# Kernel optimization log

Measured on AMD Instinct MI355X. Metric: run time of the kernel, lower is better.

## Reference

```python
import jax, jax.numpy as jnp
import numpy as np
from jax import lax

D_MODEL = 1024
EXPAND = 2
D_INNER = EXPAND * D_MODEL          # 2048
HEADDIM = 64
NHEADS = D_INNER // HEADDIM         # 32
D_STATE = 128
D_CONV = 4
NGROUPS = 1
CONV_DIM = D_INNER + 2 * NGROUPS * D_STATE   # 2304
D_IN_PROJ = 2 * D_INNER + 2 * NGROUPS * D_STATE + NHEADS  # 4384
EPS = 1e-5
BSZ, SEQ = 4, 1024


def _layer_norm(x):
    mu = jnp.mean(x, -1, keepdims=True)
    v = jnp.var(x, -1, keepdims=True)
    return (x - mu) * lax.rsqrt(v + EPS)


def _smart_flip(X, mask):
    # reverse only the non-padded prefix of each sequence
    B, L, _ = X.shape
    lengths = jnp.sum(~mask, axis=1)                     # (B,)
    r = jnp.arange(L)[None, :]                           # (1,L)
    pos = jnp.where(r < lengths[:, None], lengths[:, None] - 1 - r, r)
    return jnp.take_along_axis(X, pos[:, :, None], axis=1)


def _mamba2(u, in_proj_w, conv_w, conv_b, dt_bias, A_log, D, norm_w, out_proj_w):
    B, L, _ = u.shape
    zxbcdt = jnp.einsum('bld,ed->ble', u, in_proj_w)     # (B,L,D_IN_PROJ)
    z = zxbcdt[..., :D_INNER]
    xBC = zxbcdt[..., D_INNER:D_INNER + CONV_DIM]
    dt = zxbcdt[..., D_INNER + CONV_DIM:]                # (B,L,H)
    dt = jax.nn.softplus(dt + dt_bias)
    # causal depthwise conv1d over time, then SiLU
    xc = jnp.transpose(xBC, (0, 2, 1))                   # (B,C,L)
    xc = jnp.pad(xc, ((0, 0), (0, 0), (D_CONV - 1, 0)))
    xc = lax.conv_general_dilated(xc, conv_w.reshape(CONV_DIM, 1, D_CONV), (1,), 'VALID',
                                  feature_group_count=CONV_DIM)
    xBC = jax.nn.silu(jnp.transpose(xc + conv_b[None, :, None], (0, 2, 1)))
    x = xBC[..., :D_INNER].reshape(B, L, NHEADS, HEADDIM)
    Bmat = xBC[..., D_INNER:D_INNER + D_STATE]           # (B,L,N)  (ngroups=1)
    Cmat = xBC[..., D_INNER + D_STATE:]                  # (B,L,N)
    A = -jnp.exp(A_log)                                  # (H,)
    dA = jnp.exp(dt * A)                                 # (B,L,H)

    def step(h, inp):
        dA_t, dt_t, x_t, B_t, C_t = inp
        # h: (B,H,P,N)
        h = h * dA_t[:, :, None, None] + (dt_t[:, :, None] * x_t)[..., None] * B_t[:, None, None, :]
        y = jnp.einsum('bhpn,bn->bhp', h, C_t)
        return h, y

    h0 = jnp.zeros((B, NHEADS, HEADDIM, D_STATE), u.dtype)
    xs = (jnp.moveaxis(dA, 1, 0), jnp.moveaxis(dt, 1, 0), jnp.moveaxis(x, 1, 0),
          jnp.moveaxis(Bmat, 1, 0), jnp.moveaxis(Cmat, 1, 0))
    _, ys = lax.scan(step, h0, xs)                       # (L,B,H,P)
    y = jnp.moveaxis(ys, 0, 1) + D[None, None, :, None] * x
    y = y.reshape(B, L, D_INNER)
    g = y * jax.nn.silu(z)                               # gated RMSNorm (norm_before_gate=False)
    y = g * lax.rsqrt(jnp.mean(g * g, -1, keepdims=True) + EPS) * norm_w
    return jnp.einsum('ble,de->bld', y, out_proj_w)


def setup_inputs() -> dict:
    key = jax.random.key(0)
    ks = jax.random.split(key, 16)
    dt_f = jax.random.uniform(ks[4], (NHEADS,), minval=0.001, maxval=0.1)
    dt_r = jax.random.uniform(ks[10], (NHEADS,), minval=0.001, maxval=0.1)
    inv_softplus = lambda d: d + jnp.log(-jnp.expm1(-d))
    return {
        'hidden_states': jax.random.normal(ks[0], (BSZ, SEQ, D_MODEL), jnp.float32),
        'src_key_padding_mask': jnp.zeros((BSZ, SEQ), jnp.bool_),
        'in_proj_w': jax.random.normal(ks[1], (D_IN_PROJ, D_MODEL), jnp.float32) / np.sqrt(D_MODEL),
        'out_proj_w': jax.random.normal(ks[2], (D_MODEL, D_INNER), jnp.float32) / np.sqrt(D_INNER),
        'conv_w_f': jax.random.normal(ks[3], (CONV_DIM, D_CONV), jnp.float32) / np.sqrt(D_CONV),
        'conv_b_f': jnp.zeros((CONV_DIM,), jnp.float32),
        'dt_bias_f': inv_softplus(dt_f),
        'A_log_f': jnp.log(jax.random.uniform(ks[5], (NHEADS,), minval=1.0, maxval=16.0)),
        'D_f': jnp.ones((NHEADS,), jnp.float32),
        'norm_w_f': jnp.ones((D_INNER,), jnp.float32),
        'conv_w_r': jax.random.normal(ks[9], (CONV_DIM, D_CONV), jnp.float32) / np.sqrt(D_CONV),
        'conv_b_r': jnp.zeros((CONV_DIM,), jnp.float32),
        'dt_bias_r': inv_softplus(dt_r),
        'A_log_r': jnp.log(jax.random.uniform(ks[11], (NHEADS,), minval=1.0, maxval=16.0)),
        'D_r': jnp.ones((NHEADS,), jnp.float32),
        'norm_w_r': jnp.ones((D_INNER,), jnp.float32),
    }


def reference(hidden_states, src_key_padding_mask, in_proj_w, out_proj_w,
              conv_w_f, conv_b_f, dt_bias_f, A_log_f, D_f, norm_w_f,
              conv_w_r, conv_b_r, dt_bias_r, A_log_r, D_r, norm_w_r):
    h = _layer_norm(hidden_states)
    out = _mamba2(h, in_proj_w, conv_w_f, conv_b_f, dt_bias_f, A_log_f, D_f, norm_w_f, out_proj_w)
    rev = _smart_flip(h, src_key_padding_mask)
    out_rev = _mamba2(rev, in_proj_w, conv_w_r, conv_b_r, dt_bias_r, A_log_r, D_r, norm_w_r, out_proj_w)
    out_rev = _smart_flip(out_rev, src_key_padding_mask)
    out = (out + out_rev) / 2
    return _layer_norm(out)
```

## Files before the change

kernel.cpp:

```cpp
#include <hip/hip_runtime.h>


#define BSZ 4
#define SEQ 1024
#define DMODEL 1024
#define DINNER 2048
#define NHEADS 32
#define HEADDIM 64
#define DSTATE 128
#define CONVDIM 2304
#define DPROJ 4384
#define DPROJ_PAD 4480
#define NTOK (BSZ*SEQ)
#define EPSF 1e-5f
#define CH 32
#define NCHK (SEQ/CH)

typedef float f32x4 __attribute__((ext_vector_type(4)));
typedef __bf16 bf16x8 __attribute__((ext_vector_type(8)));
typedef __bf16 bf16x4 __attribute__((ext_vector_type(4)));

__device__ __forceinline__ unsigned short f2bf(float f) {
  unsigned int x = __float_as_uint(f);
  unsigned int r = (x + 0x7fffu + ((x >> 16) & 1u)) >> 16;
  return (unsigned short)r;
}
__device__ __forceinline__ float bf2f(unsigned short u) {
  return __uint_as_float(((unsigned int)u) << 16);
}

__device__ __forceinline__ void async_load16(const void* g, void* l) {
  __builtin_amdgcn_global_load_lds(
      (const __attribute__((address_space(1))) void*)g,
      (__attribute__((address_space(3))) void*)l, 16, 0, 0);
}

#define W1N (DPROJ_PAD * DMODEL)
#define W2N (DMODEL * DINNER)
__global__ void k_convert(const float* __restrict__ w1, const float* __restrict__ w2,
                          unsigned short* __restrict__ o1, unsigned short* __restrict__ o2) {
  int idx = blockIdx.x * 256 + threadIdx.x;
  if (idx < W1N) {
    int row = idx >> 10, col = idx & 1023;
    float v = (row < DPROJ) ? w1[(size_t)row * DMODEL + col] : 0.f;
    o1[idx] = f2bf(v);
  } else {
    int k = idx - W1N;
    o2[k] = f2bf(w2[k]);
  }
}
__global__ void k_lengths(const unsigned char* __restrict__ mask, int* __restrict__ lengths) {
  int b = blockIdx.x, tid = threadIdx.x;
  int cnt = 0;
  for (int k = 0; k < 4; ++k)
    cnt += (mask[(size_t)b * SEQ + tid + k * 256] == 0) ? 1 : 0;
  for (int o = 32; o > 0; o >>= 1) cnt += __shfl_down(cnt, o);
  __shared__ int red[4];
  if ((tid & 63) == 0) red[tid >> 6] = cnt;
  __syncthreads();
  if (tid == 0) lengths[b] = red[0] + red[1] + red[2] + red[3];
}

__global__ __launch_bounds__(256) void k_ln_bf16(const float* __restrict__ in,
                                                 unsigned short* __restrict__ out) {
  int row = blockIdx.x, tid = threadIdx.x;
  float4 v = ((const float4*)(in + (size_t)row * DMODEL))[tid];
  float s = v.x + v.y + v.z + v.w;
  float ss = v.x * v.x + v.y * v.y + v.z * v.z + v.w * v.w;
  for (int o = 32; o > 0; o >>= 1) { s += __shfl_down(s, o); ss += __shfl_down(ss, o); }
  __shared__ float red[8];
  if ((tid & 63) == 0) { red[tid >> 6] = s; red[4 + (tid >> 6)] = ss; }
  __syncthreads();
  s = red[0] + red[1] + red[2] + red[3];
  ss = red[4] + red[5] + red[6] + red[7];
  float mu = s * (1.f / DMODEL);
  float var = ss * (1.f / DMODEL) - mu * mu;
  float rs = rsqrtf(var + EPSF);
  ushort4 o;
  o.x = f2bf((v.x - mu) * rs); o.y = f2bf((v.y - mu) * rs);
  o.z = f2bf((v.z - mu) * rs); o.w = f2bf((v.w - mu) * rs);
  ((ushort4*)(out + (size_t)row * DMODEL))[tid] = o;
}

__global__ __launch_bounds__(256) void k_ln_out(const unsigned short* __restrict__ in,
                                                float* __restrict__ out) {
  int row = blockIdx.x, tid = threadIdx.x;
  ushort4 u = ((const ushort4*)(in + (size_t)row * DMODEL))[tid];
  float4 v;
  v.x = bf2f(u.x); v.y = bf2f(u.y); v.z = bf2f(u.z); v.w = bf2f(u.w);
  float s = v.x + v.y + v.z + v.w;
  float ss = v.x * v.x + v.y * v.y + v.z * v.z + v.w * v.w;
  for (int o = 32; o > 0; o >>= 1) { s += __shfl_down(s, o); ss += __shfl_down(ss, o); }
  __shared__ float red[8];
  if ((tid & 63) == 0) { red[tid >> 6] = s; red[4 + (tid >> 6)] = ss; }
  __syncthreads();
  s = red[0] + red[1] + red[2] + red[3];
  ss = red[4] + red[5] + red[6] + red[7];
  float mu = s * (1.f / DMODEL);
  float var = ss * (1.f / DMODEL) - mu * mu;
  float rs = rsqrtf(var + EPSF);
  float4 o;
  o.x = (v.x - mu) * rs; o.y = (v.y - mu) * rs;
  o.z = (v.z - mu) * rs; o.w = (v.w - mu) * rs;
  ((float4*)(out + (size_t)row * DMODEL))[tid] = o;
}

__global__ __launch_bounds__(256) void k_gemm_bt_h(const unsigned short* __restrict__ A,
                                                   const unsigned short* __restrict__ B,
                                                   unsigned short* __restrict__ C,
                                                   int K, int lda, int ldb, int ldc) {
  __shared__ unsigned short Asm[2][128 * 32];
  __shared__ unsigned short Bsm[2][128 * 32];
  const int tid = threadIdx.x;
  const int lane = tid & 63;
  const int w = tid >> 6;
  const int wm = w >> 1, wn = w & 1;
  const long m0 = (long)blockIdx.x * 128;
  const long n0 = (long)blockIdx.y * 128;

  const int sr = lane >> 2;
  const int sc = (lane & 3) * 8;
  const unsigned short* gA0 = A + (m0 + (w * 2 + 0) * 16 + sr) * (long)lda + sc;
  const unsigned short* gA1 = A + (m0 + (w * 2 + 1) * 16 + sr) * (long)lda + sc;
  const unsigned short* gB0 = B + (n0 + (w * 2 + 0) * 16 + sr) * (long)ldb + sc;
  const unsigned short* gB1 = B + (n0 + (w * 2 + 1) * 16 + sr) * (long)ldb + sc;

  f32x4 acc[4][4] = {};
  const int q8 = (lane >> 4) * 8;
  const int r16 = lane & 15;

  for (int k0 = 0; k0 < K; k0 += 64) {
#pragma unroll
    for (int h = 0; h < 2; ++h) {
      const int ko = k0 + h * 32;
      async_load16(gA0 + ko, Asm[h] + (w * 2 + 0) * 512);
      async_load16(gA1 + ko, Asm[h] + (w * 2 + 1) * 512);
      async_load16(gB0 + ko, Bsm[h] + (w * 2 + 0) * 512);
      async_load16(gB1 + ko, Bsm[h] + (w * 2 + 1) * 512);
    }
    __syncthreads();
#pragma unroll
    for (int h = 0; h < 2; ++h) {
      bf16x8 af[4], bfr[4];
#pragma unroll
      for (int i = 0; i < 4; ++i)
        af[i] = *reinterpret_cast<const bf16x8*>(Asm[h] + (wm * 64 + i * 16 + r16) * 32 + q8);
#pragma unroll
      for (int j = 0; j < 4; ++j)
        bfr[j] = *reinterpret_cast<const bf16x8*>(Bsm[h] + (wn * 64 + j * 16 + r16) * 32 + q8);
#pragma unroll
      for (int i = 0; i < 4; ++i)
#pragma unroll
        for (int j = 0; j < 4; ++j)
          acc[i][j] = __builtin_amdgcn_mfma_f32_16x16x32_bf16(af[i], bfr[j], acc[i][j], 0, 0, 0);
    }
    __syncthreads();
  }
  const int q = lane >> 4, cn = lane & 15;
#pragma unroll
  for (int i = 0; i < 4; ++i)
#pragma unroll
    for (int j = 0; j < 4; ++j) {
      long crow = m0 + wm * 64 + i * 16 + q * 4;
      long ccol = n0 + wn * 64 + j * 16 + cn;
#pragma unroll
      for (int r = 0; r < 4; ++r)
        C[(crow + r) * (long)ldc + ccol] = f2bf(acc[i][j][r]);
    }
}

__global__ __launch_bounds__(256) void k_conv(
    const __bf16* __restrict__ zxb,
    const float* __restrict__ cw_f, const float* __restrict__ cb_f,
    const float* __restrict__ cw_r, const float* __restrict__ cb_r,
    const int* __restrict__ lengths,
    __bf16* __restrict__ xb) {
  const int bx = blockIdx.x;
  const int tg = bx & 63;
  const int db = bx >> 6;
  const int b = db & 3;
  const int dir = db >> 2;
  const int tid = threadIdx.x;
  const int len = lengths[b];
  const int t0 = tg * 16;

  const float* cw = dir ? cw_r : cw_f;
  const float* cb = dir ? cb_r : cb_f;

  float w0[9], w1[9], w2[9], w3[9], bias[9];
  float r0[9], r1[9], r2[9], r3[9];
#pragma unroll
  for (int k = 0; k < 9; ++k) {
    int c = tid + k * 256;
    float4 w4 = *(const float4*)(cw + (size_t)c * 4);
    w0[k] = w4.x; w1[k] = w4.y; w2[k] = w4.z; w3[k] = w4.w;
    bias[k] = cb[c];
    r0[k] = 0.f; r1[k] = 0.f; r2[k] = 0.f;
  }
  auto rowptr = [&](int tt) -> const __bf16* {
    int s = dir ? ((tt < len) ? (len - 1 - tt) : tt) : tt;
    return zxb + ((size_t)b * SEQ + s) * DPROJ_PAD + DINNER;
  };
  if (t0 >= 3) {
    const __bf16* ra = rowptr(t0 - 3);
    const __bf16* rb = rowptr(t0 - 2);
    const __bf16* rc = rowptr(t0 - 1);
#pragma unroll
    for (int k = 0; k < 9; ++k) {
      int c = tid + k * 256;
      r0[k] = (float)ra[c]; r1[k] = (float)rb[c]; r2[k] = (float)rc[c];
    }
  }
  {
    const __bf16* rp = rowptr(t0);
#pragma unroll
    for (int k = 0; k < 9; ++k) r3[k] = (float)rp[tid + k * 256];
  }
  for (int j = 0; j < 16; ++j) {
    float r4[9];
    if (j < 15) {
      const __bf16* rp = rowptr(t0 + j + 1);
#pragma unroll
      for (int k = 0; k < 9; ++k) r4[k] = (float)rp[tid + k * 256];
    }
    __bf16* orow = xb + ((size_t)db * SEQ + t0 + j) * CONVDIM;
#pragma unroll
    for (int k = 0; k < 9; ++k) {
      float acc = bias[k];
      acc = fmaf(w0[k], r0[k], acc);
      acc = fmaf(w1[k], r1[k], acc);
      acc = fmaf(w2[k], r2[k], acc);
      acc = fmaf(w3[k], r3[k], acc);
      float sig = 1.f / (1.f + __expf(-acc));
      orow[tid + k * 256] = (__bf16)(acc * sig);
      r0[k] = r1[k]; r1[k] = r2[k]; r2[k] = r3[k]; r3[k] = r4[k];
    }
  }
}

__global__ __launch_bounds__(256) void k_dtprep(
    const __bf16* __restrict__ zxb,
    const float* __restrict__ dtb_f, const float* __restrict__ dtb_r,
    const float* __restrict__ al_f, const float* __restrict__ al_r,
    const int* __restrict__ lengths, float* __restrict__ ddg) {
  const int task = (blockIdx.x * 256 + threadIdx.x) >> 5;
  const int l32 = threadIdx.x & 31;
  const int chunk = task & 31, hh = (task >> 5) & 31, db = task >> 10;
  const int b = db & 3, dir = db >> 2;
  const int len = lengths[b];
  const float dtbv = (dir ? dtb_r : dtb_f)[hh];
  const float Ah = -__expf((dir ? al_r : al_f)[hh]);
  const int s = chunk * 32 + l32;
  const int sf = dir ? ((s < len) ? (len - 1 - s) : s) : s;
  float raw = (float)zxb[(size_t)(b * SEQ + sf) * DPROJ_PAD + DINNER + CONVDIM + hh] + dtbv;
  float d = (raw > 20.f) ? raw : log1pf(__expf(raw));
  float cum = d;
#pragma unroll
  for (int o = 1; o < 32; o <<= 1) {
    float v = __shfl_up(cum, o, 32);
    if (l32 >= o) cum += v;
  }
  float cum31 = __shfl(cum, 31, 32);
  float* o = ddg + (size_t)task * 128;
  o[l32]      = d;
  o[32 + l32] = Ah * cum;
  o[64 + l32] = d * __expf(Ah * (cum31 - cum));
  o[96 + l32] = __expf(Ah * cum);
}

__global__ __launch_bounds__(256, 2) void k_scan(
    const __bf16* __restrict__ xb, const float* __restrict__ ddg,
    const float* __restrict__ D_f, const float* __restrict__ D_r,
    unsigned short* __restrict__ y) {
  __shared__ __bf16 Crawf[4096];
  __shared__ __bf16 Brawf[4096];
  __shared__ __bf16 Braw2[4096];
  __shared__ __bf16 BTf[4096];
  __shared__ float  ddL[2][128];
  __shared__ __bf16 SL[1024];
  __shared__ __bf16 HL[4][2048];

  const int bx = blockIdx.x;
  const int h = bx & 31;
  const int db = bx >> 5;
  const int dir = db >> 2;
  const int tid = threadIdx.x;
  const int lane = tid & 63;
  const int w = tid >> 6;
  const int l15 = lane & 15;
  const int q = lane >> 4;

  const float Dh = (dir ? D_r : D_f)[h];
  const __bf16* xbase = xb + (size_t)db * SEQ * CONVDIM;
  const float* ddbase = ddg + (size_t)bx * NCHK * 128;
  unsigned short* ybase = y + (size_t)db * SEQ * DINNER + h * HEADDIM;

  for (int i = lane; i < 2048; i += 64) HL[w][i] = (__bf16)0.f;
  for (int i = tid; i < 1024; i += 256) SL[i] = (__bf16)0.f;

  f32x4 accH[8] = {};

  auto issue = [&](int c, int nb) {
    const __bf16* xr = xbase + (size_t)c * CH * CONVDIM;
#pragma unroll
    for (int k = 0; k < 2; ++k) {
      const int idx = w * 2 + k;
      const int P = idx * 64 + lane;
      const int tt = P >> 8, kk = (P >> 6) & 3, qq = (P >> 4) & 3, ll = P & 15;
      const __bf16* gB = xr + (size_t)(tt * 16 + ll) * CONVDIM + DINNER + kk * 32 + qq * 8;
      async_load16(gB, &Brawf[idx * 512]);
      async_load16(gB + 128, &Crawf[idx * 512]);
      const int s = P >> 4, n8 = P & 15;
      const __bf16* g2 = xr + (size_t)s * CONVDIM + DINNER + n8 * 8;
      async_load16(g2, &Braw2[idx * 512]);
    }
    if (w == 3 && lane < 32)
      async_load16(ddbase + (size_t)c * 128 + lane * 4, &ddL[nb][0]);
  };

  auto load_xt = [&](int c) {
    bf16x8 v;
    const __bf16* gx = xbase + (size_t)(c * CH + q * 8) * CONVDIM + h * HEADDIM + w * 16 + l15;
#pragma unroll
    for (int j = 0; j < 8; ++j) v[j] = gx[(size_t)j * CONVDIM];
    return v;
  };

  issue(0, 0);
  bf16x8 xt = load_xt(0);
  __syncthreads();

  for (int c = 0; c < NCHK; ++c) {
    const int cb = c & 1, nb = cb ^ 1;

    {
      const int n = tid & 127, sg = tid >> 7;
#pragma unroll
      for (int e = 0; e < 2; ++e) {
        const int qp = sg * 2 + e;
        bf16x8 v;
#pragma unroll
        for (int j = 0; j < 8; ++j) v[j] = Braw2[(qp * 8 + j) * 128 + n];
        *(bf16x8*)&BTf[((n >> 4) * 64 + qp * 16 + (n & 15)) * 8] = v;
      }
    }

    bf16x8 Cf0[4], Cf1[4];
#pragma unroll
    for (int kk = 0; kk < 4; ++kk) {
      Cf0[kk] = *(const bf16x8*)&Crawf[(kk * 64 + lane) * 8];
      Cf1[kk] = *(const bf16x8*)&Crawf[((4 + kk) * 64 + lane) * 8];
    }
    if (w < 3) {
      const int tt = (w == 0) ? 0 : 1;
      const int ss = (w == 2) ? 1 : 0;
      f32x4 G = {};
#pragma unroll
      for (int kk = 0; kk < 4; ++kk) {
        bf16x8 Bq = *(const bf16x8*)&Brawf[((ss * 4 + kk) * 64 + lane) * 8];
        G = __builtin_amdgcn_mfma_f32_16x16x32_bf16(Bq, tt ? Cf1[kk] : Cf0[kk], G, 0, 0, 0);
      }
      const float cdt = ddL[cb][32 + tt * 16 + l15];
      f32x4 sdt4 = *(const f32x4*)&ddL[cb][ss * 16 + q * 4];
      f32x4 cds4 = *(const f32x4*)&ddL[cb][32 + ss * 16 + q * 4];
      bf16x4 sv;
#pragma unroll
      for (int r = 0; r < 4; ++r) {
        const int s0 = q * 4 + r;
        float v = G[r] * sdt4[r] * __expf(cdt - cds4[r]);
        if (tt == ss) {
          if (l15 < s0) v = 0.f;
          else if (l15 == s0) v += Dh;
        }
        sv[r] = (__bf16)v;
      }
      *(bf16x4*)&SL[tt * 512 + (ss * 2 + (q >> 1)) * 128 + l15 * 8 + (q & 1) * 4] = sv;
    }
    __syncthreads();

    if (c + 1 < NCHK) issue(c + 1, nb);
    bf16x8 xt_n;
    if (c + 1 < NCHK) xt_n = load_xt(c + 1);

    f32x4 accy0 = {}, accy1 = {};
    {
      bf16x8 S0 = *(const bf16x8*)&SL[lane * 8];
      bf16x8 S1 = *(const bf16x8*)&SL[(64 + lane) * 8];
      accy0 = __builtin_amdgcn_mfma_f32_16x16x32_bf16(S0, xt, accy0, 0, 0, 0);
      accy1 = __builtin_amdgcn_mfma_f32_16x16x32_bf16(S1, xt, accy1, 0, 0, 0);
    }
    {
      f32x4 ai0 = {}, ai1 = {};
#pragma unroll
      for (int kk = 0; kk < 4; ++kk) {
        bf16x8 Hf = *(const bf16x8*)&HL[w][(kk * 64 + lane) * 8];
        ai0 = __builtin_amdgcn_mfma_f32_16x16x32_bf16(Cf0[kk], Hf, ai0, 0, 0, 0);
        ai1 = __builtin_amdgcn_mfma_f32_16x16x32_bf16(Cf1[kk], Hf, ai1, 0, 0, 0);
      }
      f32x4 P0 = *(const f32x4*)&ddL[cb][96 + q * 4];
      f32x4 P1 = *(const f32x4*)&ddL[cb][96 + 16 + q * 4];
      accy0 = accy0 + ai0 * P0;
      accy1 = accy1 + ai1 * P1;
    }
    {
      const float atot = ddL[cb][96 + 31];
      bf16x8 xw;
#pragma unroll
      for (int j = 0; j < 8; ++j)
        xw[j] = (__bf16)((float)xt[j] * ddL[cb][64 + q * 8 + j]);
#pragma unroll
      for (int nt = 0; nt < 8; ++nt) {
        bf16x8 Bt = *(const bf16x8*)&BTf[(nt * 64 + lane) * 8];
        accH[nt] = accH[nt] * atot;
        accH[nt] = __builtin_amdgcn_mfma_f32_16x16x32_bf16(Bt, xw, accH[nt], 0, 0, 0);
      }
#pragma unroll
      for (int nt = 0; nt < 8; ++nt) {
        const int n0 = nt * 16 + q * 4;
        bf16x4 hv;
#pragma unroll
        for (int r = 0; r < 4; ++r) hv[r] = (__bf16)accH[nt][r];
        *(bf16x4*)&HL[w][(n0 >> 5) * 512 + ((n0 >> 3) & 3) * 128 + l15 * 8 + (n0 & 7)] = hv;
      }
    }
#pragma unroll
    for (int r = 0; r < 4; ++r) {
      ybase[(size_t)(c * CH + q * 4 + r) * DINNER + w * 16 + l15] = f2bf(accy0[r]);
      ybase[(size_t)(c * CH + 16 + q * 4 + r) * DINNER + w * 16 + l15] = f2bf(accy1[r]);
    }
    xt = xt_n;
    __syncthreads();
  }
}

__global__ __launch_bounds__(256) void k_gate_combine(
    const __bf16* __restrict__ zxb, const unsigned short* __restrict__ y,
    const float* __restrict__ nw_f, const float* __restrict__ nw_r,
    const int* __restrict__ lengths, unsigned short* __restrict__ comb) {
  const int bx = blockIdx.x;
  const int b = bx >> 10, l = bx & 1023;
  const int tid = threadIdx.x;
  const int len = lengths[b];
  const int pos = (l < len) ? (len - 1 - l) : l;
  const __bf16* z = zxb + (size_t)bx * DPROJ_PAD;
  const unsigned short* yf = y + ((size_t)b * SEQ + l) * DINNER;
  const unsigned short* yr = y + ((size_t)(BSZ + b) * SEQ + pos) * DINNER;

  float gf[8], gr[8];
  float sf = 0.f, sr = 0.f;
#pragma unroll
  for (int k = 0; k < 8; ++k) {
    int c = tid + k * 256;
    float zz = (float)z[c];
    float sz = zz / (1.f + __expf(-zz));
    float vf = bf2f(yf[c]) * sz;
    float vr = bf2f(yr[c]) * sz;
    gf[k] = vf; gr[k] = vr;
    sf += vf * vf; sr += vr * vr;
  }
  for (int o = 32; o > 0; o >>= 1) { sf += __shfl_down(sf, o); sr += __shfl_down(sr, o); }
  __shared__ float red[8];
  if ((tid & 63) == 0) { red[tid >> 6] = sf; red[4 + (tid >> 6)] = sr; }
  __syncthreads();
  sf = red[0] + red[1] + red[2] + red[3];
  sr = red[4] + red[5] + red[6] + red[7];
  float rf = rsqrtf(sf * (1.f / DINNER) + EPSF);
  float rr = rsqrtf(sr * (1.f / DINNER) + EPSF);
#pragma unroll
  for (int k = 0; k < 8; ++k) {
    int c = tid + k * 256;
    float o = 0.5f * (gf[k] * rf * nw_f[c] + gr[k] * rr * nw_r[c]);
    comb[(size_t)bx * DINNER + c] = f2bf(o);
  }
}

extern "C" void kernel_launch(void* const* d_in, const int* in_sizes, int n_in,
                              void* d_out, int out_size, void* d_ws, size_t ws_size,
                              hipStream_t stream) {
  const float* hidden      = (const float*)d_in[0];
  const unsigned char* msk = (const unsigned char*)d_in[1];
  const float* in_proj_w   = (const float*)d_in[2];
  const float* out_proj_w  = (const float*)d_in[3];
  const float* conv_w_f    = (const float*)d_in[4];
  const float* conv_b_f    = (const float*)d_in[5];
  const float* dt_bias_f   = (const float*)d_in[6];
  const float* A_log_f     = (const float*)d_in[7];
  const float* D_f         = (const float*)d_in[8];
  const float* norm_w_f    = (const float*)d_in[9];
  const float* conv_w_r    = (const float*)d_in[10];
  const float* conv_b_r    = (const float*)d_in[11];
  const float* dt_bias_r   = (const float*)d_in[12];
  const float* A_log_r     = (const float*)d_in[13];
  const float* D_r         = (const float*)d_in[14];
  const float* norm_w_r    = (const float*)d_in[15];
  float* outF = (float*)d_out;

  char* ws = (char*)d_ws;
  size_t o_w1b  = 0;
  size_t o_w2b  = o_w1b  + 9175040;
  size_t o_hb   = o_w2b  + 4194304;
  size_t o_zx   = o_hb   + 8388608;
  size_t o_xb   = o_zx   + 36700160;
  size_t o_dd   = o_xb   + 37748736;
  size_t o_y    = o_dd   + 4194304;
  size_t o_comb = o_y    + 33554432;
  size_t o_outp = o_comb + 16777216;
  size_t o_len  = o_outp + 8388608;

  unsigned short* W1b  = (unsigned short*)(ws + o_w1b);
  unsigned short* W2b  = (unsigned short*)(ws + o_w2b);
  unsigned short* hb   = (unsigned short*)(ws + o_hb);
  __bf16*         zxb  = (__bf16*)(ws + o_zx);
  __bf16*         xb   = (__bf16*)(ws + o_xb);
  float*          ddg  = (float*)(ws + o_dd);
  unsigned short* yB   = (unsigned short*)(ws + o_y);
  unsigned short* comb = (unsigned short*)(ws + o_comb);
  unsigned short* outp = (unsigned short*)(ws + o_outp);
  int*            lens = (int*)(ws + o_len);

  k_convert<<<(W1N + W2N) / 256, 256, 0, stream>>>(in_proj_w, out_proj_w, W1b, W2b);
  k_lengths<<<BSZ, 256, 0, stream>>>(msk, lens);

  k_ln_bf16<<<NTOK, 256, 0, stream>>>(hidden, hb);

  k_gemm_bt_h<<<dim3(NTOK / 128, DPROJ_PAD / 128), 256, 0, stream>>>(
      hb, W1b, (unsigned short*)zxb, DMODEL, DMODEL, DMODEL, DPROJ_PAD);

  k_conv<<<2 * BSZ * (SEQ / 16), 256, 0, stream>>>(
      zxb, conv_w_f, conv_b_f, conv_w_r, conv_b_r, lens, xb);

  k_dtprep<<<1024, 256, 0, stream>>>(
      zxb, dt_bias_f, dt_bias_r, A_log_f, A_log_r, lens, ddg);

  k_scan<<<2 * BSZ * NHEADS, 256, 0, stream>>>(xb, ddg, D_f, D_r, yB);

  k_gate_combine<<<NTOK, 256, 0, stream>>>(zxb, yB, norm_w_f, norm_w_r, lens, comb);

  k_gemm_bt_h<<<dim3(NTOK / 128, DMODEL / 128), 256, 0, stream>>>(
      comb, W2b, outp, DINNER, DINNER, DINNER, DMODEL);

  k_ln_out<<<NTOK, 256, 0, stream>>>(outp, outF);

  (void)in_sizes; (void)n_in; (void)out_size; (void)ws_size;
}
```

Baseline: 308.6 us.

## Split scan state dimension across two wave groups with LDS-staged output reduction

The chunked SSM scan kernel now runs 512 threads per block. Two groups of four waves each handle half of the state dimension N, which halves the per-wave accH registers and MFMA work per chunk. Partial y outputs from each group go into double-buffered LDS tiles and are summed and written as vectorized bf16x4 stores during the next iteration. This replaces scattered scalar global stores. It adds more LDS (dynamic, about 71KB), an extra reduction step, and the loss of the two-blocks-per-CU launch bound, to raise parallelism on a grid of only 256 blocks.

```diff
diff --git a/kernel.cpp b/kernel.cpp
--- a/kernel.cpp
+++ b/kernel.cpp
@@ -268,17 +268,31 @@
   o[96 + l32] = __expf(Ah * cum);
 }
 
-__global__ __launch_bounds__(256, 2) void k_scan(
+#define SMS_CRAW 0
+#define SMS_BRAW 8192
+#define SMS_B2   16384
+#define SMS_BTF  24576
+#define SMS_DDL  32768
+#define SMS_SL   33792
+#define SMS_HL   37888
+#define SMS_YOA  54272
+#define SMS_YOB  63488
+#define SMS_TOTAL 72704
+
+__global__ __launch_bounds__(512) void k_scan(
     const __bf16* __restrict__ xb, const float* __restrict__ ddg,
     const float* __restrict__ D_f, const float* __restrict__ D_r,
     unsigned short* __restrict__ y) {
-  __shared__ __bf16 Crawf[4096];
-  __shared__ __bf16 Brawf[4096];
-  __shared__ __bf16 Braw2[4096];
-  __shared__ __bf16 BTf[4096];
-  __shared__ float  ddL[2][128];
-  __shared__ __bf16 SL[1024];
-  __shared__ __bf16 HL[4][2048];
+  extern __shared__ char smem[];
+  __bf16* const Crawf = (__bf16*)(smem + SMS_CRAW);
+  __bf16* const Brawf = (__bf16*)(smem + SMS_BRAW);
+  __bf16* const Braw2 = (__bf16*)(smem + SMS_B2);
+  __bf16* const BTf   = (__bf16*)(smem + SMS_BTF);
+  float*  const ddL   = (float*)(smem + SMS_DDL);
+  __bf16* const SL    = (__bf16*)(smem + SMS_SL);
+  __bf16* const HL    = (__bf16*)(smem + SMS_HL);
+  __bf16* const yOa   = (__bf16*)(smem + SMS_YOA);
+  __bf16* const yOb   = (__bf16*)(smem + SMS_YOB);
 
   const int bx = blockIdx.x;
   const int h = bx & 31;
@@ -287,6 +301,8 @@
   const int tid = threadIdx.x;
   const int lane = tid & 63;
   const int w = tid >> 6;
+  const int ng = w >> 2;
+  const int wl = w & 3;
   const int l15 = lane & 15;
   const int q = lane >> 4;
 
@@ -295,32 +311,32 @@
   const float* ddbase = ddg + (size_t)bx * NCHK * 128;
   unsigned short* ybase = y + (size_t)db * SEQ * DINNER + h * HEADDIM;
 
-  for (int i = lane; i < 2048; i += 64) HL[w][i] = (__bf16)0.f;
-  for (int i = tid; i < 1024; i += 256) SL[i] = (__bf16)0.f;
-
-  f32x4 accH[8] = {};
+  for (int i = tid; i < 8192; i += 512) HL[i] = (__bf16)0.f;
+  for (int i = tid; i < 2048; i += 512) SL[i] = (__bf16)0.f;
+
+  f32x4 accH[4] = {};
 
   auto issue = [&](int c, int nb) {
     const __bf16* xr = xbase + (size_t)c * CH * CONVDIM;
-#pragma unroll
-    for (int k = 0; k < 2; ++k) {
-      const int idx = w * 2 + k;
-      const int P = idx * 64 + lane;
+    const int P = w * 64 + lane;
+    {
       const int tt = P >> 8, kk = (P >> 6) & 3, qq = (P >> 4) & 3, ll = P & 15;
       const __bf16* gB = xr + (size_t)(tt * 16 + ll) * CONVDIM + DINNER + kk * 32 + qq * 8;
-      async_load16(gB, &Brawf[idx * 512]);
-      async_load16(gB + 128, &Crawf[idx * 512]);
+      async_load16(gB, &Brawf[w * 512]);
+      async_load16(gB + 128, &Crawf[w * 512]);
+    }
+    {
       const int s = P >> 4, n8 = P & 15;
       const __bf16* g2 = xr + (size_t)s * CONVDIM + DINNER + n8 * 8;
-      async_load16(g2, &Braw2[idx * 512]);
+      async_load16(g2, &Braw2[w * 512]);
     }
     if (w == 3 && lane < 32)
-      async_load16(ddbase + (size_t)c * 128 + lane * 4, &ddL[nb][0]);
+      async_load16(ddbase + (size_t)c * 128 + lane * 4, &ddL[nb * 128]);
   };
 
   auto load_xt = [&](int c) {
     bf16x8 v;
-    const __bf16* gx = xbase + (size_t)(c * CH + q * 8) * CONVDIM + h * HEADDIM + w * 16 + l15;
+    const __bf16* gx = xbase + (size_t)(c * CH + q * 8) * CONVDIM + h * HEADDIM + wl * 16 + l15;
 #pragma unroll
     for (int j = 0; j < 8; ++j) v[j] = gx[(size_t)j * CONVDIM];
     return v;
@@ -333,36 +349,42 @@
   for (int c = 0; c < NCHK; ++c) {
     const int cb = c & 1, nb = cb ^ 1;
 
+    if (c > 0) {
+      const int tf = tid >> 4, p4 = (tid & 15) * 4;
+      bf16x4 a = *(const bf16x4*)&yOa[nb * 2304 + tf * 72 + p4];
+      bf16x4 b = *(const bf16x4*)&yOb[nb * 2304 + tf * 72 + p4];
+      bf16x4 o;
+#pragma unroll
+      for (int r = 0; r < 4; ++r) o[r] = (__bf16)((float)a[r] + (float)b[r]);
+      *(bf16x4*)(ybase + (size_t)((c - 1) * CH + tf) * DINNER + p4) = o;
+    }
+
     {
       const int n = tid & 127, sg = tid >> 7;
-#pragma unroll
-      for (int e = 0; e < 2; ++e) {
-        const int qp = sg * 2 + e;
-        bf16x8 v;
-#pragma unroll
-        for (int j = 0; j < 8; ++j) v[j] = Braw2[(qp * 8 + j) * 128 + n];
-        *(bf16x8*)&BTf[((n >> 4) * 64 + qp * 16 + (n & 15)) * 8] = v;
-      }
-    }
-
-    bf16x8 Cf0[4], Cf1[4];
-#pragma unroll
-    for (int kk = 0; kk < 4; ++kk) {
-      Cf0[kk] = *(const bf16x8*)&Crawf[(kk * 64 + lane) * 8];
-      Cf1[kk] = *(const bf16x8*)&Crawf[((4 + kk) * 64 + lane) * 8];
-    }
-    if (w < 3) {
-      const int tt = (w == 0) ? 0 : 1;
-      const int ss = (w == 2) ? 1 : 0;
+      bf16x8 v;
+#pragma unroll
+      for (int j = 0; j < 8; ++j) v[j] = Braw2[(sg * 8 + j) * 128 + n];
+      *(bf16x8*)&BTf[((n >> 4) * 64 + sg * 16 + (n & 15)) * 8] = v;
+    }
+
+    bf16x8 Cf0[2], Cf1[2];
+#pragma unroll
+    for (int kk = 0; kk < 2; ++kk) {
+      Cf0[kk] = *(const bf16x8*)&Crawf[((ng * 2 + kk) * 64 + lane) * 8];
+      Cf1[kk] = *(const bf16x8*)&Crawf[((4 + ng * 2 + kk) * 64 + lane) * 8];
+    }
+    if (wl < 3) {
+      const int tt = (wl == 0) ? 0 : 1;
+      const int ss = (wl == 2) ? 1 : 0;
       f32x4 G = {};
 #pragma unroll
-      for (int kk = 0; kk < 4; ++kk) {
-        bf16x8 Bq = *(const bf16x8*)&Brawf[((ss * 4 + kk) * 64 + lane) * 8];
+      for (int kk = 0; kk < 2; ++kk) {
+        bf16x8 Bq = *(const bf16x8*)&Brawf[((ss * 4 + ng * 2 + kk) * 64 + lane) * 8];
         G = __builtin_amdgcn_mfma_f32_16x16x32_bf16(Bq, tt ? Cf1[kk] : Cf0[kk], G, 0, 0, 0);
       }
-      const float cdt = ddL[cb][32 + tt * 16 + l15];
-      f32x4 sdt4 = *(const f32x4*)&ddL[cb][ss * 16 + q * 4];
-      f32x4 cds4 = *(const f32x4*)&ddL[cb][32 + ss * 16 + q * 4];
+      const float cdt = ddL[cb * 128 + 32 + tt * 16 + l15];
+      f32x4 sdt4 = *(const f32x4*)&ddL[cb * 128 + ss * 16 + q * 4];
+      f32x4 cds4 = *(const f32x4*)&ddL[cb * 128 + 32 + ss * 16 + q * 4];
       bf16x4 sv;
 #pragma unroll
       for (int r = 0; r < 4; ++r) {
@@ -370,11 +392,11 @@
         float v = G[r] * sdt4[r] * __expf(cdt - cds4[r]);
         if (tt == ss) {
           if (l15 < s0) v = 0.f;
-          else if (l15 == s0) v += Dh;
+          else if (l15 == s0 && ng == 0) v += Dh;
         }
         sv[r] = (__bf16)v;
       }
-      *(bf16x4*)&SL[tt * 512 + (ss * 2 + (q >> 1)) * 128 + l15 * 8 + (q & 1) * 4] = sv;
+      *(bf16x4*)&SL[ng * 1024 + tt * 512 + (ss * 2 + (q >> 1)) * 128 + l15 * 8 + (q & 1) * 4] = sv;
     }
     __syncthreads();
 
@@ -384,52 +406,64 @@
 
     f32x4 accy0 = {}, accy1 = {};
     {
-      bf16x8 S0 = *(const bf16x8*)&SL[lane * 8];
-      bf16x8 S1 = *(const bf16x8*)&SL[(64 + lane) * 8];
-      accy0 = __builtin_amdgcn_mfma_f32_16x16x32_bf16(S0, xt, accy0, 0, 0, 0);
-      accy1 = __builtin_amdgcn_mfma_f32_16x16x32_bf16(S1, xt, accy1, 0, 0, 0);
+      bf16x8 S0 = *(const bf16x8*)&SL[ng * 1024 + lane * 8];
+      bf16x8 S1 = *(const bf16x8*)&SL[ng * 1024 + (64 + lane) * 8];
+      accy0 = __builtin_amdgcn_mfma_f32_16x16x32_bf16(xt, S0, accy0, 0, 0, 0);
+      accy1 = __builtin_amdgcn_mfma_f32_16x16x32_bf16(xt, S1, accy1, 0, 0, 0);
     }
     {
       f32x4 ai0 = {}, ai1 = {};
 #pragma unroll
-      for (int kk = 0; kk < 4; ++kk) {
-        bf16x8 Hf = *(const bf16x8*)&HL[w][(kk * 64 + lane) * 8];
-        ai0 = __builtin_amdgcn_mfma_f32_16x16x32_bf16(Cf0[kk], Hf, ai0, 0, 0, 0);
-        ai1 = __builtin_amdgcn_mfma_f32_16x16x32_bf16(Cf1[kk], Hf, ai1, 0, 0, 0);
+      for (int kk = 0; kk < 2; ++kk) {
+        bf16x8 Hf = *(const bf16x8*)&HL[wl * 2048 + ((ng * 2 + kk) * 64 + lane) * 8];
+        ai0 = __builtin_amdgcn_mfma_f32_16x16x32_bf16(Hf, Cf0[kk], ai0, 0, 0, 0);
+        ai1 = __builtin_amdgcn_mfma_f32_16x16x32_bf16(Hf, Cf1[kk], ai1, 0, 0, 0);
       }
-      f32x4 P0 = *(const f32x4*)&ddL[cb][96 + q * 4];
-      f32x4 P1 = *(const f32x4*)&ddL[cb][96 + 16 + q * 4];
+      const float P0 = ddL[cb * 128 + 96 + l15], P1 = ddL[cb * 128 + 96 + 16 + l15];
       accy0 = accy0 + ai0 * P0;
       accy1 = accy1 + ai1 * P1;
     }
     {
-      const float atot = ddL[cb][96 + 31];
+      const float atot = ddL[cb * 128 + 96 + 31];
       bf16x8 xw;
 #pragma unroll
       for (int j = 0; j < 8; ++j)
-        xw[j] = (__bf16)((float)xt[j] * ddL[cb][64 + q * 8 + j]);
-#pragma unroll
-      for (int nt = 0; nt < 8; ++nt) {
-        bf16x8 Bt = *(const bf16x8*)&BTf[(nt * 64 + lane) * 8];
+        xw[j] = (__bf16)((float)xt[j] * ddL[cb * 128 + 64 + q * 8 + j]);
+#pragma unroll
+      for (int nt = 0; nt < 4; ++nt) {
+        bf16x8 Bt = *(const bf16x8*)&BTf[((ng * 4 + nt) * 64 + lane) * 8];
         accH[nt] = accH[nt] * atot;
         accH[nt] = __builtin_amdgcn_mfma_f32_16x16x32_bf16(Bt, xw, accH[nt], 0, 0, 0);
       }
 #pragma unroll
-      for (int nt = 0; nt < 8; ++nt) {
-        const int n0 = nt * 16 + q * 4;
+      for (int nt = 0; nt < 4; ++nt) {
+        const int n0 = (ng * 4 + nt) * 16 + q * 4;
         bf16x4 hv;
 #pragma unroll
         for (int r = 0; r < 4; ++r) hv[r] = (__bf16)accH[nt][r];
-        *(bf16x4*)&HL[w][(n0 >> 5) * 512 + ((n0 >> 3) & 3) * 128 + l15 * 8 + (n0 & 7)] = hv;
+        *(bf16x4*)&HL[wl * 2048 + (n0 >> 5) * 512 + ((n0 >> 3) & 3) * 128 + l15 * 8 + (n0 & 7)] = hv;
       }
     }
-#pragma unroll
-    for (int r = 0; r < 4; ++r) {
-      ybase[(size_t)(c * CH + q * 4 + r) * DINNER + w * 16 + l15] = f2bf(accy0[r]);
-      ybase[(size_t)(c * CH + 16 + q * 4 + r) * DINNER + w * 16 + l15] = f2bf(accy1[r]);
+    {
+      __bf16* yO = (ng ? yOb : yOa) + cb * 2304;
+      bf16x4 v0, v1;
+#pragma unroll
+      for (int r = 0; r < 4; ++r) { v0[r] = (__bf16)accy0[r]; v1[r] = (__bf16)accy1[r]; }
+      *(bf16x4*)&yO[l15 * 72 + wl * 16 + q * 4] = v0;
+      *(bf16x4*)&yO[(16 + l15) * 72 + wl * 16 + q * 4] = v1;
     }
     xt = xt_n;
     __syncthreads();
+  }
+  {
+    const int tf = tid >> 4, p4 = (tid & 15) * 4;
+    const int lb = (NCHK - 1) & 1;
+    bf16x4 a = *(const bf16x4*)&yOa[lb * 2304 + tf * 72 + p4];
+    bf16x4 b = *(const bf16x4*)&yOb[lb * 2304 + tf * 72 + p4];
+    bf16x4 o;
+#pragma unroll
+    for (int r = 0; r < 4; ++r) o[r] = (__bf16)((float)a[r] + (float)b[r]);
+    *(bf16x4*)(ybase + (size_t)((NCHK - 1) * CH + tf) * DINNER + p4) = o;
   }
 }
 
@@ -518,6 +552,13 @@
   unsigned short* outp = (unsigned short*)(ws + o_outp);
   int*            lens = (int*)(ws + o_len);
 
+  static bool s_attr_done = false;
+  if (!s_attr_done) {
+    hipFuncSetAttribute(reinterpret_cast<const void*>(k_scan),
+                        hipFuncAttributeMaxDynamicSharedMemorySize, SMS_TOTAL);
+    s_attr_done = true;
+  }
+
   k_convert<<<(W1N + W2N) / 256, 256, 0, stream>>>(in_proj_w, out_proj_w, W1b, W2b);
   k_lengths<<<BSZ, 256, 0, stream>>>(msk, lens);
 
@@ -532,7 +573,7 @@
   k_dtprep<<<1024, 256, 0, stream>>>(
       zxb, dt_bias_f, dt_bias_r, A_log_f, A_log_r, lens, ddg);
 
-  k_scan<<<2 * BSZ * NHEADS, 256, 0, stream>>>(xb, ddg, D_f, D_r, yB);
+  k_scan<<<2 * BSZ * NHEADS, 512, SMS_TOTAL, stream>>>(xb, ddg, D_f, D_r, yB);
 
   k_gate_combine<<<NTOK, 256, 0, stream>>>(zxb, yB, norm_w_f, norm_w_r, lens, comb);
 
```

Result: no change. 312.8 us (+1.4%).
